# Performance work log

Hardware: AMD Instinct MI355X
Metric: run time of the kernel (lower is better)

## Reference

```python
import jax, jax.numpy as jnp
import numpy as np

B, S, D, H = 2, 512, 512, 8
HD = D // H  # 64


def setup_inputs() -> dict:
    key = jax.random.key(0)
    ks = jax.random.split(key, 14)
    sd = 1.0 / np.sqrt(D)
    sh = 1.0 / np.sqrt(HD)
    return {
        "query": jax.random.normal(ks[0], (B, S, D), jnp.float32),
        "key_": jax.random.normal(ks[1], (B, S, D), jnp.float32),
        "value": jax.random.normal(ks[2], (B, S, D), jnp.float32),
        "Wq": jax.random.uniform(ks[3], (D, D), jnp.float32, -sd, sd),
        "bq": jax.random.uniform(ks[4], (D,), jnp.float32, -sd, sd),
        "Wk": jax.random.uniform(ks[5], (D, D), jnp.float32, -sd, sd),
        "bk": jax.random.uniform(ks[6], (D,), jnp.float32, -sd, sd),
        "Wv": jax.random.uniform(ks[7], (D, D), jnp.float32, -sd, sd),
        "bv": jax.random.uniform(ks[8], (D,), jnp.float32, -sd, sd),
        "Wo": jax.random.uniform(ks[9], (D, D), jnp.float32, -sd, sd),
        "bo": jax.random.uniform(ks[10], (D,), jnp.float32, -sd, sd),
        "Aq": jax.random.uniform(ks[11], (HD, HD), jnp.float32, -sh, sh),
        "Ak": jax.random.uniform(ks[12], (HD, HD), jnp.float32, -sh, sh),
        "av": jax.random.normal(ks[13], (HD,), jnp.float32) * sh,
    }


def _heads(x):
    b, s, _ = x.shape
    return x.reshape(b, s, H, HD).transpose(0, 2, 1, 3)  # [b,h,s,hd]


def reference(query, key_, value, Wq, bq, Wk, bk, Wv, bv, Wo, bo, Aq, Ak, av):
    q = _heads(query @ Wq + bq)   # [b,h,q,hd]
    k = _heads(key_ @ Wk + bk)    # [b,h,k,hd]
    v = _heads(value @ Wv + bv)   # [b,h,k,hd]
    # additive (Bahdanau-style) scores: tanh(add_q(q)[:,:,:,None]+add_k(k)[:,:,None]) . av
    q_term = (q @ Aq)[:, :, :, None, :]   # [b,h,q,1,hd]
    k_term = (k @ Ak)[:, :, None, :, :]   # [b,h,1,k,hd]
    scores = jnp.einsum('bhqkd,d->bhqk', jnp.tanh(q_term + k_term), av)
    attn_weights = jax.nn.softmax(scores, axis=-1)  # dropout is identity at eval
    ctx = jnp.einsum('bhqk,bhkd->bhqd', attn_weights, v)
    b, _, s, _ = ctx.shape
    ctx = ctx.transpose(0, 2, 1, 3).reshape(b, s, D)
    out = ctx @ Wo + bo
    return out, attn_weights
```

## Files before the change

kernel.cpp:

```cpp
#include <hip/hip_runtime.h>
#include <math.h>

#define Bb 2
#define Ss 512
#define Dd 512
#define Hh 8
#define HDd 64
#define BS (Bb*Ss)

#if __has_builtin(__builtin_amdgcn_exp2f)
#define EXP2F(x) __builtin_amdgcn_exp2f(x)
#else
#define EXP2F(x) exp2f(x)
#endif
#if __has_builtin(__builtin_amdgcn_rcpf)
#define RCPF(x) __builtin_amdgcn_rcpf(x)
#else
#define RCPF(x) (1.0f/(x))
#endif

typedef float v4f __attribute__((ext_vector_type(4)));
typedef short v8s __attribute__((ext_vector_type(8)));

struct HL { short h, l; };

__device__ __forceinline__ HL split1(float x) {
  unsigned u = __builtin_bit_cast(unsigned, x);
  unsigned h = (u + 0x7fffu + ((u >> 16) & 1u)) >> 16;
  float hf = __builtin_bit_cast(float, h << 16);
  float lo = x - hf;
  unsigned ul = __builtin_bit_cast(unsigned, lo);
  unsigned l = (ul + 0x7fffu + ((ul >> 16) & 1u)) >> 16;
  HL r; r.h = (short)h; r.l = (short)l;
  return r;
}

__device__ __forceinline__ void split8p(const float* __restrict__ xp, v8s& ah, v8s& al) {
#pragma unroll
  for (int j = 0; j < 8; j++) {
    const HL r = split1(xp[j]);
    ah[j] = r.h; al[j] = r.l;
  }
}

__device__ __forceinline__ void split8v(float4 x0, float4 x1, v8s& ah, v8s& al) {
  HL r;
  r = split1(x0.x); ah[0] = r.h; al[0] = r.l;
  r = split1(x0.y); ah[1] = r.h; al[1] = r.l;
  r = split1(x0.z); ah[2] = r.h; al[2] = r.l;
  r = split1(x0.w); ah[3] = r.h; al[3] = r.l;
  r = split1(x1.x); ah[4] = r.h; al[4] = r.l;
  r = split1(x1.y); ah[5] = r.h; al[5] = r.l;
  r = split1(x1.z); ah[6] = r.h; al[6] = r.l;
  r = split1(x1.w); ah[7] = r.h; al[7] = r.l;
}

#if __has_builtin(__builtin_amdgcn_global_load_lds)
__device__ __forceinline__ void gl2lds16(const float* g, float* l) {
  __builtin_amdgcn_global_load_lds(
      (const __attribute__((address_space(1))) void*)g,
      (__attribute__((address_space(3))) void*)l, 16, 0, 0);
}
#else
__device__ __forceinline__ void gl2lds16(const float* g, float* l) {
  const int lane = threadIdx.x & 63;
  *(float4*)((char*)l + lane * 16) = *(const float4*)g;
}
#endif

__global__ __launch_bounds__(256) void qkv_all(
    const float* __restrict__ Xq, const float* __restrict__ Xk, const float* __restrict__ Xv,
    const float* __restrict__ Wq, const float* __restrict__ Wk, const float* __restrict__ Wv,
    const float* __restrict__ Wo,
    const float* __restrict__ bq, const float* __restrict__ bk, const float* __restrict__ bv,
    const float* __restrict__ Aq, const float* __restrict__ Ak,
    float* __restrict__ EQ, float* __restrict__ EKt, float* __restrict__ Vw,
    short* __restrict__ WoPk)
{
  __shared__ __align__(16) short fragH[2][4][64][8];
  __shared__ __align__(16) short fragL[2][4][64][8];
  __shared__ float qs[64][68];
  __shared__ float qs2[16][260];

  const int z = blockIdx.z;
  const float* X    = (z == 0) ? Xq : (z == 1) ? Xk : Xv;
  const float* W    = (z == 0) ? Wq : (z == 1) ? Wk : Wv;
  const float* bias = (z == 0) ? bq : (z == 1) ? bk : bv;
  const int tid = threadIdx.x, l = tid & 63, w = tid >> 6;
  const int lm = l & 15, lq = l >> 4;
  const int h = blockIdx.x;
  const int r0 = blockIdx.y * 64;

  v4f acc[4] = {{0.f,0.f,0.f,0.f},{0.f,0.f,0.f,0.f},{0.f,0.f,0.f,0.f},{0.f,0.f,0.f,0.f}};
  const float* xrow = X + (size_t)(r0 + w * 16 + lm) * Dd + lq * 8;

  for (int kt = 0; kt < 16; ++kt) {
    const int buf = kt & 1;
    const float4 xa0 = *(const float4*)&xrow[kt * 32];
    const float4 xa1 = *(const float4*)&xrow[kt * 32 + 4];
    {
      v8s hh, ll;
#pragma unroll
      for (int j = 0; j < 8; j++) {
        const float x = W[(size_t)(kt * 32 + lq * 8 + j) * Dd + h * 64 + w * 16 + lm];
        const HL r = split1(x);
        hh[j] = r.h; ll[j] = r.l;
      }
      *(v8s*)&fragH[buf][w][l][0] = hh;
      *(v8s*)&fragL[buf][w][l][0] = ll;
    }
    __syncthreads();
    v8s ah, al;
    split8v(xa0, xa1, ah, al);
#pragma unroll
    for (int t = 0; t < 4; t++) {
      const v8s bh = *(const v8s*)&fragH[buf][t][l][0];
      const v8s bl = *(const v8s*)&fragL[buf][t][l][0];
      acc[t] = __builtin_amdgcn_mfma_f32_16x16x32_bf16(ah, bh, acc[t], 0, 0, 0);
      acc[t] = __builtin_amdgcn_mfma_f32_16x16x32_bf16(ah, bl, acc[t], 0, 0, 0);
      acc[t] = __builtin_amdgcn_mfma_f32_16x16x32_bf16(al, bh, acc[t], 0, 0, 0);
    }
  }

  if (z == 2) {
#pragma unroll
    for (int t = 0; t < 4; t++) {
      const int n = h * 64 + t * 16 + lm;
      const float bvv = bias[n];
#pragma unroll
      for (int r = 0; r < 4; r++)
        Vw[(size_t)(r0 + w * 16 + lq * 4 + r) * Dd + n] = acc[t][r] + bvv;
    }
    {
      const int tau = (blockIdx.y * 8 + h) * 4 + w;
      const int nt = tau >> 4, kt = tau & 15;
      v8s hh, ll;
#pragma unroll
      for (int j = 0; j < 8; j++) {
        const float x = Wo[(size_t)(kt * 32 + lq * 8 + j) * Dd + nt * 16 + lm];
        const HL r = split1(x);
        hh[j] = r.h; ll[j] = r.l;
      }
      *(v8s*)&WoPk[((size_t)tau * 64 + l) * 16 + 0] = hh;
      *(v8s*)&WoPk[((size_t)tau * 64 + l) * 16 + 8] = ll;
    }
    return;
  }

#pragma unroll
  for (int t = 0; t < 4; t++) {
    const int n = h * 64 + t * 16 + lm;
    const float bvv = bias[n];
#pragma unroll
    for (int r = 0; r < 4; r++)
      qs[w * 16 + lq * 4 + r][t * 16 + lm] = acc[t][r] + bvv;
  }
  __syncthreads();

  const float* Am = (z == 0) ? Aq : Ak;
  v4f a2[4] = {{0.f,0.f,0.f,0.f},{0.f,0.f,0.f,0.f},{0.f,0.f,0.f,0.f},{0.f,0.f,0.f,0.f}};
#pragma unroll
  for (int kt2 = 0; kt2 < 2; ++kt2) {
    v8s ah, al;
    split8p(&qs[w * 16 + lm][kt2 * 32 + lq * 8], ah, al);
#pragma unroll
    for (int t2 = 0; t2 < 4; t2++) {
      v8s bh, bl;
#pragma unroll
      for (int j = 0; j < 8; j++) {
        const float x = Am[(kt2 * 32 + lq * 8 + j) * HDd + t2 * 16 + lm]
                        * 2.885390081777927f;
        const HL r = split1(x);
        bh[j] = r.h; bl[j] = r.l;
      }
      a2[t2] = __builtin_amdgcn_mfma_f32_16x16x32_bf16(ah, bh, a2[t2], 0, 0, 0);
      a2[t2] = __builtin_amdgcn_mfma_f32_16x16x32_bf16(ah, bl, a2[t2], 0, 0, 0);
      a2[t2] = __builtin_amdgcn_mfma_f32_16x16x32_bf16(al, bh, a2[t2], 0, 0, 0);
    }
  }

  if (z == 0) {
#pragma unroll
    for (int t2 = 0; t2 < 4; t2++)
#pragma unroll
      for (int rr = 0; rr < 4; rr++)
        EQ[(size_t)(r0 + w * 16 + lq * 4 + rr) * Dd + h * 64 + t2 * 16 + lm] = EXP2F(a2[t2][rr]);
  } else {
#pragma unroll
    for (int t2 = 0; t2 < 4; t2++)
#pragma unroll
      for (int rr = 0; rr < 4; rr++)
        qs2[4 * t2 + (lm >> 2)][(w * 16 + lq * 4 + rr) * 4 + (lm & 3)] = EXP2F(a2[t2][rr]);
    __syncthreads();
    const int b = r0 >> 9;
    const size_t base = (size_t)(b * 8 + h) * 16 * 2048 + (size_t)(r0 & 511) * 4;
#pragma unroll
    for (int i = 0; i < 4; i++) {
      const int f = i * 1024 + tid * 4;
      const int dt = f >> 8, c = f & 255;
      *(float4*)&EKt[base + (size_t)dt * 2048 + c] = *(const float4*)&qs2[dt][c];
    }
  }
}

__device__ __forceinline__ float grp4(v4f e, v4f ek, v4f av4) {
  const v4f one = {1.f, 1.f, 1.f, 1.f};
  const v4f den = e * ek + one;
  const float AB = den.x * den.y;
  const float CD = den.z * den.w;
  const float n1 = __builtin_fmaf(av4.y, den.x, av4.x * den.y);
  const float n2 = __builtin_fmaf(av4.w, den.z, av4.z * den.w);
  const float N = __builtin_fmaf(n2, AB, n1 * CD);
  return N * RCPF(AB * CD);
}

__global__ __launch_bounds__(256) void attn_kernel(
    const float* __restrict__ EQ, const float* __restrict__ EKt,
    const float* __restrict__ V, const float* __restrict__ av,
    float* __restrict__ attnW, float* __restrict__ CTX)
{
  __shared__ __align__(16) float uni[8256];
  __shared__ __align__(16) float eq_s[16][64];
  __shared__ float avn[64];

  const int tid = threadIdx.x, l = tid & 63, w = tid >> 6;
  const int q0 = blockIdx.x * 16;
  const int bh = blockIdx.y;
  const int b = bh >> 3, h = bh & 7;

  {
    const float* eqg = EQ + (size_t)(b * Ss + q0 + w * 4 + (l >> 4)) * Dd
                       + h * HDd + (l & 15) * 4;
    gl2lds16(eqg, &eq_s[w * 4][0]);
  }
  if (tid < 64) avn[tid] = -2.f * av[tid];

  const float* ekbase = EKt + (size_t)bh * 16 * 2048;
  gl2lds16(ekbase + w * 512 + l * 4, &uni[w * 512]);
  gl2lds16(ekbase + w * 512 + 256 + l * 4, &uni[w * 512 + 256]);
  __syncthreads();

  const int qg = w * 4;
  float a[4][8];
#pragma unroll
  for (int j = 0; j < 4; j++)
#pragma unroll
    for (int kg = 0; kg < 8; kg++) a[j][kg] = 0.f;

#pragma unroll 1
  for (int dt = 0; dt < 16; ++dt) {
    const int cb = (dt & 1) * 2048;
    const int nb = 2048 - cb;
    const int dtn = (dt < 15) ? dt + 1 : 15;
    gl2lds16(ekbase + (size_t)dtn * 2048 + w * 512 + l * 4, &uni[nb + w * 512]);
    gl2lds16(ekbase + (size_t)dtn * 2048 + w * 512 + 256 + l * 4, &uni[nb + w * 512 + 256]);

    const v4f av4 = *(const v4f*)&avn[dt * 4];
    const v4f e0 = *(const v4f*)&eq_s[qg + 0][dt * 4];
    const v4f e1 = *(const v4f*)&eq_s[qg + 1][dt * 4];
    const v4f e2 = *(const v4f*)&eq_s[qg + 2][dt * 4];
    const v4f e3 = *(const v4f*)&eq_s[qg + 3][dt * 4];
#pragma unroll
    for (int kg = 0; kg < 8; kg++) {
      const v4f ek = *(const v4f*)&uni[cb + kg * 256 + l * 4];
      a[0][kg] += grp4(e0, ek, av4);
      a[1][kg] += grp4(e1, ek, av4);
      a[2][kg] += grp4(e2, ek, av4);
      a[3][kg] += grp4(e3, ek, av4);
    }
    __syncthreads();
  }

#pragma unroll
  for (int j = 0; j < 4; j++) {
    float m = -1e30f;
#pragma unroll
    for (int kg = 0; kg < 8; kg++) m = fmaxf(m, a[j][kg]);
#pragma unroll
    for (int off = 32; off >= 1; off >>= 1) m = fmaxf(m, __shfl_xor(m, off, 64));
    float s = 0.f;
#pragma unroll
    for (int kg = 0; kg < 8; kg++) {
      a[j][kg] = EXP2F((a[j][kg] - m) * 1.4426950408889634f);
      s += a[j][kg];
    }
#pragma unroll
    for (int off = 32; off >= 1; off >>= 1) s += __shfl_xor(s, off, 64);
    const float inv = RCPF(s);
    float* arow = attnW + ((size_t)bh * Ss + q0 + qg + j) * Ss;
#pragma unroll
    for (int kg = 0; kg < 8; kg++) {
      const float wv = a[j][kg] * inv;
      uni[(qg + j) * 516 + kg * 64 + l] = wv;
      arow[kg * 64 + l] = wv;
    }
  }
  __syncthreads();

  {
    const int cq = tid >> 4;
    const int dq = (tid & 15) * 4;
    const float* vb = V + (size_t)b * Ss * Dd + h * HDd + dq;
    const float* scr = &uni[cq * 516];
    v4f o = {0.f, 0.f, 0.f, 0.f};
    for (int kk = 0; kk < Ss; kk += 2) {
      const float2 wv = *(const float2*)&scr[kk];
      const v4f v0 = *(const v4f*)&vb[(size_t)kk * Dd];
      const v4f v1 = *(const v4f*)&vb[(size_t)(kk + 1) * Dd];
      o += wv.x * v0 + wv.y * v1;
    }
    *(v4f*)&CTX[(size_t)(b * Ss + q0 + cq) * Dd + h * HDd + dq] = o;
  }
}

__global__ __launch_bounds__(256) void out_pk(
    const float* __restrict__ CTX, const short* __restrict__ WoPk,
    const float* __restrict__ bo, float* __restrict__ out)
{
  const int tid = threadIdx.x;
  const int l = tid & 63, w = tid >> 6;
  const int lm = l & 15, lq = l >> 4;
  const int m0 = blockIdx.y * 64 + w * 16;
  const int nt0 = blockIdx.x * 4;

  v4f acc[4] = {{0.f,0.f,0.f,0.f},{0.f,0.f,0.f,0.f},{0.f,0.f,0.f,0.f},{0.f,0.f,0.f,0.f}};
  const float* xrow = CTX + (size_t)(m0 + lm) * Dd + lq * 8;

#pragma unroll 2
  for (int kt = 0; kt < 16; ++kt) {
    v8s ah, al;
    split8p(xrow + kt * 32, ah, al);
#pragma unroll
    for (int t = 0; t < 4; t++) {
      const int tau = (nt0 + t) * 16 + kt;
      const size_t bi = ((size_t)tau * 64 + l) * 16;
      const v8s bh = *(const v8s*)&WoPk[bi + 0];
      const v8s bl = *(const v8s*)&WoPk[bi + 8];
      acc[t] = __builtin_amdgcn_mfma_f32_16x16x32_bf16(ah, bh, acc[t], 0, 0, 0);
      acc[t] = __builtin_amdgcn_mfma_f32_16x16x32_bf16(ah, bl, acc[t], 0, 0, 0);
      acc[t] = __builtin_amdgcn_mfma_f32_16x16x32_bf16(al, bh, acc[t], 0, 0, 0);
    }
  }
#pragma unroll
  for (int t = 0; t < 4; t++) {
    const int n = (nt0 + t) * 16 + lm;
    const float bv = bo[n];
#pragma unroll
    for (int r = 0; r < 4; r++)
      out[(size_t)(m0 + lq * 4 + r) * Dd + n] = acc[t][r] + bv;
  }
}

extern "C" void kernel_launch(void* const* d_in, const int* in_sizes, int n_in,
                              void* d_out, int out_size, void* d_ws, size_t ws_size,
                              hipStream_t stream) {
  (void)in_sizes; (void)n_in; (void)out_size; (void)ws_size;
  const float* query = (const float*)d_in[0];
  const float* key_  = (const float*)d_in[1];
  const float* value = (const float*)d_in[2];
  const float* Wq    = (const float*)d_in[3];
  const float* bq    = (const float*)d_in[4];
  const float* Wk    = (const float*)d_in[5];
  const float* bk    = (const float*)d_in[6];
  const float* Wv    = (const float*)d_in[7];
  const float* bv    = (const float*)d_in[8];
  const float* Wo    = (const float*)d_in[9];
  const float* bo    = (const float*)d_in[10];
  const float* Aq    = (const float*)d_in[11];
  const float* Ak    = (const float*)d_in[12];
  const float* av    = (const float*)d_in[13];

  float* outp = (float*)d_out;
  float* attn = outp + (size_t)BS * Dd;

  float* ws  = (float*)d_ws;
  float* EQ  = ws;
  float* EKt = ws + (size_t)BS * Dd;
  float* Vw  = ws + 2 * (size_t)BS * Dd;
  float* CTX = ws + 3 * (size_t)BS * Dd;
  short* WoPk = (short*)(ws + 4 * (size_t)BS * Dd);

  qkv_all<<<dim3(8, 16, 3), 256, 0, stream>>>(query, key_, value,
      Wq, Wk, Wv, Wo, bq, bk, bv, Aq, Ak, EQ, EKt, Vw, WoPk);
  attn_kernel<<<dim3(32, 16), 256, 0, stream>>>(EQ, EKt, Vw, av, attn, CTX);
  out_pk<<<dim3(8, 16), 256, 0, stream>>>(CTX, WoPk, bo, outp);
}
```

Baseline: 173.4 us.

## Fuse output projection into attention kernel with atomic accumulation across heads

Removes the separate out_pk launch. Each attention block now keeps its 16x64 context tile in shared memory and multiplies it by its head's slice of Wo using split-bf16 MFMA. It then atomically adds the partial result into the output, which qkv_all pre-fills with the bias. This saves a kernel launch and the CTX round trip through global memory, at the cost of 8-way float atomics per output element and a nondeterministic summation order.

```diff
diff --git a/kernel.cpp b/kernel.cpp
--- a/kernel.cpp
+++ b/kernel.cpp
@@ -73,9 +73,10 @@
     const float* __restrict__ Wq, const float* __restrict__ Wk, const float* __restrict__ Wv,
     const float* __restrict__ Wo,
     const float* __restrict__ bq, const float* __restrict__ bk, const float* __restrict__ bv,
+    const float* __restrict__ bo,
     const float* __restrict__ Aq, const float* __restrict__ Ak,
     float* __restrict__ EQ, float* __restrict__ EKt, float* __restrict__ Vw,
-    short* __restrict__ WoPk)
+    short* __restrict__ WoPk, float* __restrict__ outp)
 {
   __shared__ __align__(16) short fragH[2][4][64][8];
   __shared__ __align__(16) short fragL[2][4][64][8];
@@ -143,6 +144,10 @@
       }
       *(v8s*)&WoPk[((size_t)tau * 64 + l) * 16 + 0] = hh;
       *(v8s*)&WoPk[((size_t)tau * 64 + l) * 16 + 8] = ll;
+    }
+    for (int i = tid; i < 4096; i += 256) {
+      const int rr2 = i >> 6, cc = i & 63;
+      outp[(size_t)(r0 + rr2) * Dd + h * 64 + cc] = bo[h * 64 + cc];
     }
     return;
   }
@@ -217,20 +222,22 @@
 __global__ __launch_bounds__(256) void attn_kernel(
     const float* __restrict__ EQ, const float* __restrict__ EKt,
     const float* __restrict__ V, const float* __restrict__ av,
-    float* __restrict__ attnW, float* __restrict__ CTX)
+    const short* __restrict__ WoPk,
+    float* __restrict__ attnW, float* __restrict__ outp)
 {
   __shared__ __align__(16) float uni[8256];
   __shared__ __align__(16) float eq_s[16][64];
   __shared__ float avn[64];
 
   const int tid = threadIdx.x, l = tid & 63, w = tid >> 6;
+  const int lm = l & 15, lq = l >> 4;
   const int q0 = blockIdx.x * 16;
   const int bh = blockIdx.y;
   const int b = bh >> 3, h = bh & 7;
 
   {
-    const float* eqg = EQ + (size_t)(b * Ss + q0 + w * 4 + (l >> 4)) * Dd
-                       + h * HDd + (l & 15) * 4;
+    const float* eqg = EQ + (size_t)(b * Ss + q0 + w * 4 + lq) * Dd
+                       + h * HDd + lm * 4;
     gl2lds16(eqg, &eq_s[w * 4][0]);
   }
   if (tid < 64) avn[tid] = -2.f * av[tid];
@@ -309,45 +316,36 @@
       const v4f v1 = *(const v4f*)&vb[(size_t)(kk + 1) * Dd];
       o += wv.x * v0 + wv.y * v1;
     }
-    *(v4f*)&CTX[(size_t)(b * Ss + q0 + cq) * Dd + h * HDd + dq] = o;
-  }
-}
-
-__global__ __launch_bounds__(256) void out_pk(
-    const float* __restrict__ CTX, const short* __restrict__ WoPk,
-    const float* __restrict__ bo, float* __restrict__ out)
-{
-  const int tid = threadIdx.x;
-  const int l = tid & 63, w = tid >> 6;
-  const int lm = l & 15, lq = l >> 4;
-  const int m0 = blockIdx.y * 64 + w * 16;
-  const int nt0 = blockIdx.x * 4;
-
-  v4f acc[4] = {{0.f,0.f,0.f,0.f},{0.f,0.f,0.f,0.f},{0.f,0.f,0.f,0.f},{0.f,0.f,0.f,0.f}};
-  const float* xrow = CTX + (size_t)(m0 + lm) * Dd + lq * 8;
-
-#pragma unroll 2
-  for (int kt = 0; kt < 16; ++kt) {
-    v8s ah, al;
-    split8p(xrow + kt * 32, ah, al);
-#pragma unroll
-    for (int t = 0; t < 4; t++) {
-      const int tau = (nt0 + t) * 16 + kt;
-      const size_t bi = ((size_t)tau * 64 + l) * 16;
-      const v8s bh = *(const v8s*)&WoPk[bi + 0];
-      const v8s bl = *(const v8s*)&WoPk[bi + 8];
-      acc[t] = __builtin_amdgcn_mfma_f32_16x16x32_bf16(ah, bh, acc[t], 0, 0, 0);
-      acc[t] = __builtin_amdgcn_mfma_f32_16x16x32_bf16(ah, bl, acc[t], 0, 0, 0);
-      acc[t] = __builtin_amdgcn_mfma_f32_16x16x32_bf16(al, bh, acc[t], 0, 0, 0);
-    }
-  }
-#pragma unroll
-  for (int t = 0; t < 4; t++) {
-    const int n = (nt0 + t) * 16 + lm;
-    const float bv = bo[n];
-#pragma unroll
-    for (int r = 0; r < 4; r++)
-      out[(size_t)(m0 + lq * 4 + r) * Dd + n] = acc[t][r] + bv;
+    *(v4f*)&eq_s[cq][dq] = o;
+  }
+  __syncthreads();
+
+  {
+    v4f oacc[8];
+#pragma unroll
+    for (int i = 0; i < 8; i++) oacc[i] = (v4f){0.f, 0.f, 0.f, 0.f};
+#pragma unroll
+    for (int kt2 = 0; kt2 < 2; ++kt2) {
+      v8s ah, al;
+      split8p(&eq_s[lm][kt2 * 32 + lq * 8], ah, al);
+#pragma unroll
+      for (int n8 = 0; n8 < 8; n8++) {
+        const int tau = (w * 8 + n8) * 16 + 2 * h + kt2;
+        const size_t bi = ((size_t)tau * 64 + l) * 16;
+        const v8s bh = *(const v8s*)&WoPk[bi + 0];
+        const v8s bl = *(const v8s*)&WoPk[bi + 8];
+        oacc[n8] = __builtin_amdgcn_mfma_f32_16x16x32_bf16(ah, bh, oacc[n8], 0, 0, 0);
+        oacc[n8] = __builtin_amdgcn_mfma_f32_16x16x32_bf16(ah, bl, oacc[n8], 0, 0, 0);
+        oacc[n8] = __builtin_amdgcn_mfma_f32_16x16x32_bf16(al, bh, oacc[n8], 0, 0, 0);
+      }
+    }
+#pragma unroll
+    for (int n8 = 0; n8 < 8; n8++) {
+      const int n = (w * 8 + n8) * 16 + lm;
+#pragma unroll
+      for (int r = 0; r < 4; r++)
+        atomicAdd(&outp[(size_t)(b * Ss + q0 + lq * 4 + r) * Dd + n], oacc[n8][r]);
+    }
   }
 }
 
@@ -377,11 +375,10 @@
   float* EQ  = ws;
   float* EKt = ws + (size_t)BS * Dd;
   float* Vw  = ws + 2 * (size_t)BS * Dd;
-  float* CTX = ws + 3 * (size_t)BS * Dd;
-  short* WoPk = (short*)(ws + 4 * (size_t)BS * Dd);
+  short* WoPk = (short*)(ws + 3 * (size_t)BS * Dd);
 
   qkv_all<<<dim3(8, 16, 3), 256, 0, stream>>>(query, key_, value,
-      Wq, Wk, Wv, Wo, bq, bk, bv, Aq, Ak, EQ, EKt, Vw, WoPk);
-  attn_kernel<<<dim3(32, 16), 256, 0, stream>>>(EQ, EKt, Vw, av, attn, CTX);
-  out_pk<<<dim3(8, 16), 256, 0, stream>>>(CTX, WoPk, bo, outp);
-}
+      Wq, Wk, Wv, Wo, bq, bk, bv, bo, Aq, Ak, EQ, EKt, Vw, WoPk, outp);
+  attn_kernel<<<dim3(32, 16), 256, 0, stream>>>(EQ, EKt, Vw, av,
+      WoPk, attn, outp);
+}
```

Result: no change. 170.8 us (-1.5%).
